# Performance work log

Measured on AMD Instinct MI355X. Metric: run time of the kernel, lower is better.

Reference implementation:

```python
import jax, jax.numpy as jnp
import numpy as np

N, L, V, D, E, NL = 50000, 32, 5000, 128, 800000, 3
P, B = 5000, 64

def setup_inputs() -> dict:
    key = jax.random.key(0)
    ks = jax.random.split(key, 6)
    x = jax.random.randint(ks[0], (N, L), 0, V)            # token ids, 0 = pad
    edge_index = jax.random.randint(ks[1], (2, E), 0, N)   # [2,E] src,dst
    pool_idx = jnp.arange(N) // (N // P)                   # node -> pooled supernode
    node_batch = pool_idx * B // P                         # node -> graph id (grouped, as in torch loop)
    embed = jax.random.normal(ks[2], (V, D), jnp.float32) * 0.02
    W_l = jax.random.normal(ks[3], (NL, D, D), jnp.float32) / np.sqrt(D)
    W_r = jax.random.normal(ks[4], (NL, D, D), jnp.float32) / np.sqrt(D)
    b = jnp.zeros((NL, D), jnp.float32)
    return dict(x=x, edge_index=edge_index, pool_idx=pool_idx, node_batch=node_batch,
                num_pooled=P, embed=embed, W_l=W_l, W_r=W_r, b=b)

def reference(x, edge_index, pool_idx, node_batch, num_pooled, embed, W_l, W_r, b):
    n = x.shape[0]
    dt = embed.dtype
    # masked mean-pool of token embeddings (pad id = 0), length clamped to >=1
    mask = (x != 0)
    lengths = jnp.clip(mask.sum(axis=1), 1, None).astype(dt)          # [N]
    h = (embed[x] * mask[..., None].astype(dt)).sum(axis=1) / lengths[:, None]  # [N,D]
    src, dst = edge_index[0], edge_index[1]
    deg = jnp.clip(jax.ops.segment_sum(jnp.ones(src.shape[0], dt), dst, num_segments=n), 1.0, None)
    # SAGEConv layers: mean-aggregate neighbors, lin_l(agg)+bias + lin_r(self), relu
    # (dropout p=0.5 is identity in eval mode)
    for i in range(W_l.shape[0]):
        agg = jax.ops.segment_sum(h[src], dst, num_segments=n) / deg[:, None]
        h = jax.nn.relu(agg @ W_l[i] + b[i] + h @ W_r[i])
    # global mean pool over supernodes
    cnt = jnp.clip(jax.ops.segment_sum(jnp.ones(n, dt), pool_idx, num_segments=num_pooled), 1.0, None)
    x_pooled = jax.ops.segment_sum(h, pool_idx, num_segments=num_pooled) / cnt[:, None]
    # global max pool of graph ids -> pooled batch vector
    batch_pooled = jax.ops.segment_max(node_batch, pool_idx, num_segments=num_pooled)
    # coalesced pooled edges without self-loops, as a dense boolean adjacency
    sp, dp = pool_idx[src], pool_idx[dst]
    adj = jnp.zeros((num_pooled, num_pooled), jnp.bool_).at[sp, dp].set(True)
    adj = adj & ~jnp.eye(num_pooled, dtype=jnp.bool_)
    return x_pooled, adj, batch_pooled
```

## Files before the change

kernel.cpp:

```cpp
#include <hip/hip_runtime.h>
#include <limits.h>

#define D 128

typedef __attribute__((ext_vector_type(8))) short bf16x8;
typedef __attribute__((ext_vector_type(4))) float f32x4;

static __device__ __forceinline__ unsigned short f2bf(float f) {
    unsigned u = __builtin_bit_cast(unsigned, f);
    u += 0x7FFFu + ((u >> 16) & 1u);
    return (unsigned short)(u >> 16);
}
static __device__ __forceinline__ float bf2f(unsigned u16) {
    unsigned u = u16 << 16;
    return __builtin_bit_cast(float, u);
}
static __device__ __forceinline__ bf16x8 load_frag(const unsigned short* p) {
    uint4 v = *(const uint4*)p;
    return __builtin_bit_cast(bf16x8, v);
}
static __device__ __forceinline__ void acc8(float* a, uint4 v) {
    a[0] += bf2f(v.x & 0xffff); a[1] += bf2f(v.x >> 16);
    a[2] += bf2f(v.y & 0xffff); a[3] += bf2f(v.y >> 16);
    a[4] += bf2f(v.z & 0xffff); a[5] += bf2f(v.z >> 16);
    a[6] += bf2f(v.w & 0xffff); a[7] += bf2f(v.w >> 16);
}
static __device__ __forceinline__ ushort4 pack4(const float* a, float s) {
    ushort4 o;
    o.x = f2bf(a[0] * s); o.y = f2bf(a[1] * s);
    o.z = f2bf(a[2] * s); o.w = f2bf(a[3] * s);
    return o;
}

__global__ __launch_bounds__(256) void zero_k(float4* __restrict__ b, size_t nb)
{
    size_t i = (size_t)blockIdx.x * 256 + threadIdx.x;
    if (i < nb) b[i] = make_float4(0.f, 0.f, 0.f, 0.f);
}

__global__ __launch_bounds__(256) void epack_k(
    const float* __restrict__ embed, unsigned short* __restrict__ e16, int n4)
{
    int i = blockIdx.x * 256 + threadIdx.x;
    if (i >= n4) return;
    float4 v = *(const float4*)&embed[(size_t)i * 4];
    ushort4 o;
    o.x = f2bf(v.x); o.y = f2bf(v.y); o.z = f2bf(v.z); o.w = f2bf(v.w);
    *(ushort4*)&e16[(size_t)i * 4] = o;
}

__global__ __launch_bounds__(256) void embed_pool_k(
    const int* __restrict__ x, const unsigned short* __restrict__ e16,
    unsigned short* __restrict__ h16, int n, int L)
{
    __shared__ int toks[16][32];
    int t = threadIdx.x;
    int sub = t >> 4, s = t & 15;
    int node = blockIdx.x * 16 + sub;
    for (int j = t; j < 16 * L; j += 256) {
        int nd = blockIdx.x * 16 + j / L;
        toks[j / L][j % L] = (nd < n) ? x[(size_t)nd * L + (j % L)] : 0;
    }
    __syncthreads();
    if (node >= n) return;
    float acc[8] = {};
    int cnt = 0;
    for (int l = 0; l < L; ++l) {
        int tok = toks[sub][l];
        if (tok != 0) {
            acc8(acc, *(const uint4*)&e16[(size_t)tok * D + s * 8]);
            cnt++;
        }
    }
    float inv = 1.0f / (float)(cnt > 0 ? cnt : 1);
    ushort4 lo = pack4(acc, inv), hi = pack4(acc + 4, inv);
    *(ushort4*)&h16[(size_t)node * D + s * 8]     = lo;
    *(ushort4*)&h16[(size_t)node * D + s * 8 + 4] = hi;
}

__global__ __launch_bounds__(256) void wpack_k(
    const float* __restrict__ Wl, const float* __restrict__ Wr,
    unsigned short* __restrict__ Wp, int NL)
{
    int idx = blockIdx.x * 256 + threadIdx.x;
    if (idx >= NL * 2 * 16384) return;
    int m = idx >> 14;
    int r = idx & 16383;
    int j = r & 7;
    int lane = (r >> 3) & 63;
    int cb = (r >> 9) & 7;
    int kb = (r >> 12) & 3;
    const float* W = ((m & 1) ? Wr : Wl) + (size_t)(m >> 1) * D * D;
    int k = kb * 32 + (lane >> 4) * 8 + j;
    int c = cb * 16 + (lane & 15);
    Wp[idx] = f2bf(W[(size_t)k * D + c]);
}

__global__ __launch_bounds__(256) void deg_k(
    const int* __restrict__ ei, int* __restrict__ deg, int E)
{
    int e = blockIdx.x * 256 + threadIdx.x;
    if (e >= E) return;
    atomicAdd(&deg[ei[E + e]], 1);
}

__global__ __launch_bounds__(256) void scan_partial_k(
    const int* __restrict__ deg, int* __restrict__ bsum, int n)
{
    int b = blockIdx.x, t = threadIdx.x;
    int i0 = b * 1024 + t * 4;
    int s = 0;
    #pragma unroll
    for (int k = 0; k < 4; ++k) { int i = i0 + k; if (i < n) s += deg[i]; }
    for (int off = 32; off > 0; off >>= 1) s += __shfl_down(s, off, 64);
    __shared__ int sm4[4];
    if ((t & 63) == 0) sm4[t >> 6] = s;
    __syncthreads();
    if (t == 0) bsum[b] = sm4[0] + sm4[1] + sm4[2] + sm4[3];
}

__global__ __launch_bounds__(256) void scan_bsum_k(
    const int* __restrict__ bsum, int* __restrict__ boff, int nb)
{
    __shared__ int sm[256];
    int t = threadIdx.x;
    sm[t] = (t < nb) ? bsum[t] : 0;
    __syncthreads();
    for (int off = 1; off < 256; off <<= 1) {
        int add = (t >= off) ? sm[t - off] : 0;
        __syncthreads();
        sm[t] += add;
        __syncthreads();
    }
    if (t < nb) boff[t] = (t > 0) ? sm[t - 1] : 0;
}

__global__ __launch_bounds__(256) void scan_final_k(
    const int* __restrict__ deg, const int* __restrict__ boff,
    int* __restrict__ rp, int n)
{
    __shared__ int sm[256];
    int b = blockIdx.x, t = threadIdx.x;
    int i0 = b * 1024 + t * 4;
    int v[4];
    #pragma unroll
    for (int k = 0; k < 4; ++k) { int i = i0 + k; v[k] = (i < n) ? deg[i] : 0; }
    v[1] += v[0]; v[2] += v[1]; v[3] += v[2];
    sm[t] = v[3];
    __syncthreads();
    for (int off = 1; off < 256; off <<= 1) {
        int add = (t >= off) ? sm[t - off] : 0;
        __syncthreads();
        sm[t] += add;
        __syncthreads();
    }
    int base = boff[b] + ((t > 0) ? sm[t - 1] : 0);
    if (b == 0 && t == 0) rp[0] = 0;
    #pragma unroll
    for (int k = 0; k < 4; ++k) {
        int i = i0 + k;
        if (i < n) rp[i + 1] = base + v[k];
    }
}

__global__ __launch_bounds__(256) void edge_pass2_k(
    const int* __restrict__ ei, const int* __restrict__ rp,
    const int* __restrict__ pool, int* __restrict__ cur,
    int* __restrict__ col, float* __restrict__ adj, int E, int P)
{
    int e = blockIdx.x * 256 + threadIdx.x;
    if (e >= E) return;
    int src = ei[e], dst = ei[E + e];
    int pos = atomicAdd(&cur[dst], 1);
    col[rp[dst] + pos] = src;
    int sp = pool[src], dp = pool[dst];
    if (sp != dp) adj[(size_t)sp * P + dp] = 1.0f;
}

__global__ __launch_bounds__(256) void aggregate_k(
    const unsigned short* __restrict__ h16, const int* __restrict__ rp,
    const int* __restrict__ col, unsigned short* __restrict__ agg16, int n)
{
    int node = blockIdx.x * 4 + (threadIdx.x >> 6);
    int lane = threadIdx.x & 63;
    if (node >= n) return;
    int beg = rp[node], end = rp[node + 1];
    int q = lane >> 4, s = lane & 15;
    float acc[8] = {};
    int e = beg + q;
    for (; e + 4 < end; e += 8) {
        int s0 = col[e], s1 = col[e + 4];
        uint4 v0 = *(const uint4*)&h16[(size_t)s0 * D + s * 8];
        uint4 v1 = *(const uint4*)&h16[(size_t)s1 * D + s * 8];
        acc8(acc, v0);
        acc8(acc, v1);
    }
    if (e < end)
        acc8(acc, *(const uint4*)&h16[(size_t)col[e] * D + s * 8]);
    #pragma unroll
    for (int k = 0; k < 8; ++k) {
        acc[k] += __shfl_xor(acc[k], 16, 64);
        acc[k] += __shfl_xor(acc[k], 32, 64);
    }
    if (q == 0) {
        int dg = end - beg;
        float inv = 1.0f / (float)(dg > 0 ? dg : 1);
        ushort4 lo = pack4(acc, inv), hi = pack4(acc + 4, inv);
        *(ushort4*)&agg16[(size_t)node * D + s * 8]     = lo;
        *(ushort4*)&agg16[(size_t)node * D + s * 8 + 4] = hi;
    }
}

__global__ __launch_bounds__(256) void sage_gemm_mfma_k(
    const unsigned short* __restrict__ agg16, unsigned short* __restrict__ h16,
    const unsigned short* __restrict__ Wp,
    const float* __restrict__ bias, int n)
{
    int t = threadIdx.x;
    int w = t >> 6, lane = t & 63;
    int node0 = blockIdx.x * 128 + w * 32;
    int row = lane & 15, g = lane >> 4;

    f32x4 acc[2][8];
    #pragma unroll
    for (int i = 0; i < 2; ++i)
        #pragma unroll
        for (int c = 0; c < 8; ++c)
            acc[i][c] = (f32x4){0.f, 0.f, 0.f, 0.f};

    float bs[8];
    #pragma unroll
    for (int cb = 0; cb < 8; ++cb) bs[cb] = bias[cb * 16 + row];

    bool ok0 = (node0 < n);
    bool ok1 = (node0 + 16 < n);

    #pragma unroll
    for (int kb = 0; kb < 8; ++kb) {
        const unsigned short* Asrc = (kb < 4) ? agg16 : h16;
        int ko = (kb & 3) * 32 + g * 8;
        bf16x8 a0 = (bf16x8){0,0,0,0,0,0,0,0};
        bf16x8 a1 = a0;
        if (ok0) a0 = load_frag(&Asrc[(size_t)(node0 + row) * D + ko]);
        if (ok1) a1 = load_frag(&Asrc[(size_t)(node0 + 16 + row) * D + ko]);
        const unsigned short* wp = Wp + ((kb < 4) ? 0 : 16384) + (size_t)(kb & 3) * 4096;
        #pragma unroll
        for (int cb = 0; cb < 8; ++cb) {
            bf16x8 b = load_frag(&wp[(cb * 64 + lane) * 8]);
            acc[0][cb] = __builtin_amdgcn_mfma_f32_16x16x32_bf16(a0, b, acc[0][cb], 0, 0, 0);
            acc[1][cb] = __builtin_amdgcn_mfma_f32_16x16x32_bf16(a1, b, acc[1][cb], 0, 0, 0);
        }
    }

    #pragma unroll
    for (int rg = 0; rg < 2; ++rg) {
        int nb = node0 + rg * 16;
        if (nb >= n) break;
        #pragma unroll
        for (int cb = 0; cb < 8; ++cb) {
            int c = cb * 16 + row;
            #pragma unroll
            for (int j = 0; j < 4; ++j) {
                int node = nb + g * 4 + j;
                float v = fmaxf(acc[rg][cb][j] + bs[cb], 0.f);
                h16[(size_t)node * D + c] = f2bf(v);
            }
        }
    }
}

__global__ __launch_bounds__(128) void poolmean_k(
    const unsigned short* __restrict__ h16, const int* __restrict__ pool,
    const int* __restrict__ nbatch, float* __restrict__ outx,
    float* __restrict__ outb, int n, int P)
{
    int p = blockIdx.x;
    int d = threadIdx.x;
    int lo = 0, hi = n;
    while (lo < hi) { int mid = (lo + hi) >> 1; if (pool[mid] < p) lo = mid + 1; else hi = mid; }
    int s = lo;
    hi = n;
    while (lo < hi) { int mid = (lo + hi) >> 1; if (pool[mid] < p + 1) lo = mid + 1; else hi = mid; }
    int e = lo;
    float sum = 0.f;
    for (int i = s; i < e; ++i) sum += bf2f(h16[(size_t)i * D + d]);
    int c = e - s;
    outx[(size_t)p * D + d] = sum / (float)(c > 0 ? c : 1);
    if (d == 0) {
        int bm = INT_MIN;
        for (int i = s; i < e; ++i) bm = max(bm, nbatch[i]);
        outb[p] = (float)bm;
    }
}

extern "C" void kernel_launch(void* const* d_in, const int* in_sizes, int n_in,
                              void* d_out, int out_size, void* d_ws, size_t ws_size,
                              hipStream_t stream)
{
    const int*   x      = (const int*)d_in[0];
    const int*   ei     = (const int*)d_in[1];
    const int*   pool   = (const int*)d_in[2];
    const int*   nbatch = (const int*)d_in[3];
    const float* embed  = (const float*)d_in[5];
    const float* Wl     = (const float*)d_in[6];
    const float* Wr     = (const float*)d_in[7];
    const float* bias   = (const float*)d_in[8];

    const int N  = in_sizes[2];
    const int L  = in_sizes[0] / N;
    const int E  = in_sizes[1] / 2;
    const int VD = in_sizes[5];
    const int NL = in_sizes[6] / (D * D);
    const int P  = 5000;

    float* out_x   = (float*)d_out;
    float* out_adj = out_x + (size_t)P * D;
    float* out_b   = out_adj + (size_t)P * P;

    char* w = (char*)d_ws;
    auto alloc = [&](size_t bytes) { void* p = w; w += (bytes + 255) & ~255ULL; return p; };
    size_t ND = (size_t)N * D;
    unsigned short* h16   = (unsigned short*)alloc(ND * 2);
    unsigned short* agg16 = (unsigned short*)alloc(ND * 2);
    unsigned short* Wp    = (unsigned short*)alloc((size_t)NL * 2 * 16384 * 2);
    unsigned short* e16   = (unsigned short*)alloc((size_t)VD * 2);
    int*   col  = (int*)alloc((size_t)E * 4);
    int*   rp   = (int*)alloc((size_t)(N + 1) * 4);
    int*   bsum = (int*)alloc(256 * 4);
    int*   boff = (int*)alloc(256 * 4);
    int*   deg  = (int*)alloc((size_t)N * 2 * 4);
    int*   cur  = deg + N;

    const int NB = (N + 1023) / 1024;

    size_t nb = (size_t)N * 2 / 4;
    zero_k<<<(int)((nb + 255) / 256), 256, 0, stream>>>((float4*)deg, nb);

    epack_k<<<(VD / 4 + 255) / 256, 256, 0, stream>>>(embed, e16, VD / 4);
    wpack_k<<<(NL * 2 * 16384 + 255) / 256, 256, 0, stream>>>(Wl, Wr, Wp, NL);
    embed_pool_k<<<(N + 15) / 16, 256, 0, stream>>>(x, e16, h16, N, L);
    deg_k<<<(E + 255) / 256, 256, 0, stream>>>(ei, deg, E);
    scan_partial_k<<<NB, 256, 0, stream>>>(deg, bsum, N);
    scan_bsum_k<<<1, 256, 0, stream>>>(bsum, boff, NB);
    scan_final_k<<<NB, 256, 0, stream>>>(deg, boff, rp, N);
    edge_pass2_k<<<(E + 255) / 256, 256, 0, stream>>>(ei, rp, pool, cur, col, out_adj, E, P);

    for (int ly = 0; ly < NL; ++ly) {
        aggregate_k<<<(N + 3) / 4, 256, 0, stream>>>(h16, rp, col, agg16, N);
        sage_gemm_mfma_k<<<(N + 127) / 128, 256, 0, stream>>>(
            agg16, h16, Wp + (size_t)ly * 2 * 16384, bias + (size_t)ly * D, N);
    }

    poolmean_k<<<P, 128, 0, stream>>>(h16, pool, nbatch, out_x, out_b, N, P);
}
```

Baseline: 276.4 us.

## Bucket pooled-adjacency writes by address range before scattering to dense matrix

Instead of writing each pooled edge straight into the 100MB dense adjacency at random addresses, edges are counted into 768 address buckets (32K-entry ranges) in the degree pass, scanned together with node degrees, scattered into a key buffer, and then written by one block per bucket. This localises the dense writes so each block touches a contiguous region of the adjacency, improving cache/DRAM locality. It adds a shared-memory histogram, an extra key buffer, extra atomics and one more kernel launch.

```diff
diff --git a/kernel.cpp b/kernel.cpp
--- a/kernel.cpp
+++ b/kernel.cpp
@@ -2,6 +2,7 @@
 #include <limits.h>
 
 #define D 128
+#define NBK 768
 
 typedef __attribute__((ext_vector_type(8))) short bf16x8;
 typedef __attribute__((ext_vector_type(4))) float f32x4;
@@ -96,12 +97,28 @@
     Wp[idx] = f2bf(W[(size_t)k * D + c]);
 }
 
-__global__ __launch_bounds__(256) void deg_k(
-    const int* __restrict__ ei, int* __restrict__ deg, int E)
-{
-    int e = blockIdx.x * 256 + threadIdx.x;
-    if (e >= E) return;
-    atomicAdd(&deg[ei[E + e]], 1);
+__global__ __launch_bounds__(256) void deghist_k(
+    const int* __restrict__ ei, const int* __restrict__ pool,
+    int* __restrict__ degall, int E, int n, int P)
+{
+    __shared__ int hist[NBK];
+    int t = threadIdx.x;
+    for (int i = t; i < NBK; i += 256) hist[i] = 0;
+    __syncthreads();
+    int base = blockIdx.x * 8192;
+    for (int i = 0; i < 32; ++i) {
+        int e = base + i * 256 + t;
+        if (e >= E) break;
+        int src = ei[e], dst = ei[E + e];
+        atomicAdd(&degall[dst], 1);
+        int sp = pool[src], dp = pool[dst];
+        if (sp != dp) atomicAdd(&hist[(sp * P + dp) >> 15], 1);
+    }
+    __syncthreads();
+    for (int i = t; i < NBK; i += 256) {
+        int v = hist[i];
+        if (v) atomicAdd(&degall[n + i], v);
+    }
 }
 
 __global__ __launch_bounds__(256) void scan_partial_k(
@@ -164,17 +181,33 @@
 }
 
 __global__ __launch_bounds__(256) void edge_pass2_k(
-    const int* __restrict__ ei, const int* __restrict__ rp,
-    const int* __restrict__ pool, int* __restrict__ cur,
-    int* __restrict__ col, float* __restrict__ adj, int E, int P)
+    const int* __restrict__ ei, const int* __restrict__ rpall,
+    const int* __restrict__ pool, int* __restrict__ cur, int* __restrict__ bcur,
+    int* __restrict__ col, int* __restrict__ kbuf, int E, int n, int P)
 {
     int e = blockIdx.x * 256 + threadIdx.x;
     if (e >= E) return;
     int src = ei[e], dst = ei[E + e];
     int pos = atomicAdd(&cur[dst], 1);
-    col[rp[dst] + pos] = src;
+    col[rpall[dst] + pos] = src;
     int sp = pool[src], dp = pool[dst];
-    if (sp != dp) adj[(size_t)sp * P + dp] = 1.0f;
+    if (sp != dp) {
+        int key = sp * P + dp;
+        int b = key >> 15;
+        int kpos = atomicAdd(&bcur[b], 1);
+        kbuf[(rpall[n + b] - E) + kpos] = key;
+    }
+}
+
+__global__ __launch_bounds__(256) void adj_write_k(
+    const int* __restrict__ rpall, const int* __restrict__ kbuf,
+    float* __restrict__ adj, int E, int n)
+{
+    int b = blockIdx.x;
+    int s = rpall[n + b] - E;
+    int e = rpall[n + b + 1] - E;
+    for (int i = s + threadIdx.x; i < e; i += 256)
+        adj[(size_t)kbuf[i]] = 1.0f;
 }
 
 __global__ __launch_bounds__(256) void aggregate_k(
@@ -324,29 +357,34 @@
     unsigned short* agg16 = (unsigned short*)alloc(ND * 2);
     unsigned short* Wp    = (unsigned short*)alloc((size_t)NL * 2 * 16384 * 2);
     unsigned short* e16   = (unsigned short*)alloc((size_t)VD * 2);
-    int*   col  = (int*)alloc((size_t)E * 4);
-    int*   rp   = (int*)alloc((size_t)(N + 1) * 4);
-    int*   bsum = (int*)alloc(256 * 4);
-    int*   boff = (int*)alloc(256 * 4);
-    int*   deg  = (int*)alloc((size_t)N * 2 * 4);
-    int*   cur  = deg + N;
-
-    const int NB = (N + 1023) / 1024;
-
-    size_t nb = (size_t)N * 2 / 4;
-    zero_k<<<(int)((nb + 255) / 256), 256, 0, stream>>>((float4*)deg, nb);
+    int*   col    = (int*)alloc((size_t)E * 4);
+    int*   kbuf   = (int*)alloc((size_t)E * 4);
+    int*   rpall  = (int*)alloc((size_t)(N + NBK + 1) * 4);
+    int*   bsum   = (int*)alloc(256 * 4);
+    int*   boff   = (int*)alloc(256 * 4);
+    int*   degall = (int*)alloc((size_t)(N + NBK + N + NBK) * 4);
+    int*   cur    = degall + N + NBK;
+    int*   bcur   = cur + N;
+
+    const int NS = N + NBK;
+    const int NB = (NS + 1023) / 1024;
+
+    size_t nz = ((size_t)(N + NBK) * 2 + 3) / 4;
+    zero_k<<<(int)((nz + 255) / 256), 256, 0, stream>>>((float4*)degall, nz);
 
     epack_k<<<(VD / 4 + 255) / 256, 256, 0, stream>>>(embed, e16, VD / 4);
     wpack_k<<<(NL * 2 * 16384 + 255) / 256, 256, 0, stream>>>(Wl, Wr, Wp, NL);
     embed_pool_k<<<(N + 15) / 16, 256, 0, stream>>>(x, e16, h16, N, L);
-    deg_k<<<(E + 255) / 256, 256, 0, stream>>>(ei, deg, E);
-    scan_partial_k<<<NB, 256, 0, stream>>>(deg, bsum, N);
+    deghist_k<<<(E + 8191) / 8192, 256, 0, stream>>>(ei, pool, degall, E, N, P);
+    scan_partial_k<<<NB, 256, 0, stream>>>(degall, bsum, NS);
     scan_bsum_k<<<1, 256, 0, stream>>>(bsum, boff, NB);
-    scan_final_k<<<NB, 256, 0, stream>>>(deg, boff, rp, N);
-    edge_pass2_k<<<(E + 255) / 256, 256, 0, stream>>>(ei, rp, pool, cur, col, out_adj, E, P);
+    scan_final_k<<<NB, 256, 0, stream>>>(degall, boff, rpall, NS);
+    edge_pass2_k<<<(E + 255) / 256, 256, 0, stream>>>(
+        ei, rpall, pool, cur, bcur, col, kbuf, E, N, P);
+    adj_write_k<<<NBK, 256, 0, stream>>>(rpall, kbuf, out_adj, E, N);
 
     for (int ly = 0; ly < NL; ++ly) {
-        aggregate_k<<<(N + 3) / 4, 256, 0, stream>>>(h16, rp, col, agg16, N);
+        aggregate_k<<<(N + 3) / 4, 256, 0, stream>>>(h16, rpall, col, agg16, N);
         sage_gemm_mfma_k<<<(N + 127) / 128, 256, 0, stream>>>(
             agg16, h16, Wp + (size_t)ly * 2 * 16384, bias + (size_t)ly * D, N);
     }
```

Result: slower. 479.0 us (+73.3%).
